# Optimization experiments

Hardware: AMD Instinct MI355X
Metric: run time of the kernel (lower is better)

## Reference

```python
import jax, jax.numpy as jnp
import numpy as np
from jax import lax

B, S, HDIM = 4, 2048, 1024
H, D, L = 16, 64, 128
NB = S // L
EPS = 1e-8


def setup_inputs() -> dict:
    key = jax.random.key(0)
    ks = jax.random.split(key, 16)
    std = 0.02
    inp = {
        'f_in': jax.random.normal(ks[0], (B, S, HDIM), jnp.float32),
        'i_in': jax.random.normal(ks[1], (B, S, HDIM), jnp.float32),
        'z_in': jax.random.normal(ks[2], (B, S, HDIM), jnp.float32),
        'o_in': jax.random.normal(ks[3], (B, S, HDIM), jnp.float32),
        'c0': jax.random.normal(ks[4], (B, H, D), jnp.float32),
        'h0': jax.random.normal(ks[5], (B, H, D), jnp.float32),
        # weights stored (in, out) so forward is x @ W + b
        'Wf': std * jax.random.normal(ks[6], (HDIM, H * D), jnp.float32),
        'bf': jnp.zeros((H * D,), jnp.float32),
        'Wi': std * jax.random.normal(ks[7], (HDIM, H * D), jnp.float32),
        'bi': jnp.zeros((H * D,), jnp.float32),
        'Wz': std * jax.random.normal(ks[8], (HDIM, H * D), jnp.float32),
        'bz': jnp.zeros((H * D,), jnp.float32),
        'Wo': std * jax.random.normal(ks[9], (HDIM, H * D), jnp.float32),
        'bo': jnp.zeros((H * D,), jnp.float32),
        'Wp': std * jax.random.normal(ks[10], (H * D, HDIM), jnp.float32),
        'bp': jnp.zeros((HDIM,), jnp.float32),
    }
    return inp


def _to_blocks(x):
    # (B,S,H*D) -> (NB, B, H, D, L), matching torch view+permute(1,0,3,4,2)
    return jnp.transpose(x.reshape(B, NB, L, H, D), (1, 0, 3, 4, 2))


def _qlstm(f_in, i_in, z_in, o_in, c0, Wf, bf, Wi, bi, Wz, bz, Wo, bo, Wp, bp):
    fx = _to_blocks(f_in @ Wf + bf)
    ix = _to_blocks(i_in @ Wi + bi)
    zx = _to_blocks(z_in @ Wz + bz)
    ox = _to_blocks(o_in @ Wo + bo)

    f = jax.nn.sigmoid(fx + 1.0)              # (NB,B,H,D,L)
    o = jax.nn.sigmoid(ox)
    update = jax.nn.sigmoid(ix) * jnp.tanh(zx)

    kk = jnp.arange(L)[:, None]
    ll = jnp.arange(L + 1)[None, :]
    ones_mask = ll >= kk + 1                   # (L, L+1): filled with 1.0
    zeros_mask = ll >= kk + 2                  # (L, L+1): zeroed out

    def block_step(c, blk):
        fb, ob, ub = blk                       # each (B,H,D,L)
        cf = jnp.concatenate([fb, jnp.ones(fb.shape[:-1] + (1,), fb.dtype)], axis=-1)  # (B,H,D,L+1)
        Fm = jnp.broadcast_to(cf[..., None, :], fb.shape[:-1] + (L, L + 1))
        Fm = jnp.where(ones_mask, 1.0, Fm)
        # reversed log-cumsum-exp along last axis (decay products)
        Fm = jnp.exp(jnp.flip(jnp.cumsum(jnp.flip(jnp.log(Fm + EPS), -1), -1), -1)) - EPS
        Fm = jnp.where(zeros_mask, 0.0, Fm)    # (B,H,D,L,L+1)
        u = jnp.concatenate([c[..., None], ub], axis=-1)   # (B,H,D,L+1)
        cs = jnp.einsum('bhdkl,bhdl->bhdk', Fm, u)          # (B,H,D,L)
        hs = ob * jnp.tanh(cs)
        return cs[..., -1], hs

    last_c, hs = lax.scan(block_step, c0, (f, o, update))   # hs: (NB,B,H,D,L)
    last_h = hs[-1, ..., -1]
    y = jnp.transpose(hs, (1, 0, 4, 2, 3)).reshape(B, S, H * D)
    y = y @ Wp + bp                            # (B,S,HDIM)
    return y, last_c, last_h


def reference(f_in, i_in, z_in, o_in, c0, h0, Wf, bf, Wi, bi, Wz, bz, Wo, bo, Wp, bp):
    y, last_c, last_h = _qlstm(f_in, i_in, z_in, o_in, c0,
                               Wf, bf, Wi, bi, Wz, bz, Wo, bo, Wp, bp)
    return y, last_c, last_h
```

## Files before the change

kernel.cpp:

```cpp
#include <hip/hip_runtime.h>
#include <hip/hip_bf16.h>
#include <stdint.h>

constexpr int GM = 8192;
constexpr int GK = 1024;
constexpr int GN = 1024;
constexpr size_t NACT = (size_t)GM * GN;
constexpr int CHUNK = 32;
constexpr int NCHUNK = 64;
constexpr int NCH = 4096;

#define DEVINL __device__ __forceinline__

typedef __attribute__((ext_vector_type(8))) short bf16x8;
typedef __attribute__((ext_vector_type(4))) float f32x4;

DEVINL float sigmoidf_(float x) { return 1.0f / (1.0f + __expf(-x)); }

DEVINL unsigned short f2bf(float x) {
  unsigned int u = __builtin_bit_cast(unsigned int, x);
  unsigned int rnd = 0x7fffu + ((u >> 16) & 1u);
  return (unsigned short)((u + rnd) >> 16);
}
DEVINL float bf2f(unsigned short u) {
  unsigned int x = ((unsigned int)u) << 16;
  return __builtin_bit_cast(float, x);
}

DEVINL void gload16(const void* g, void* l) {
  __builtin_amdgcn_global_load_lds(
      (const __attribute__((address_space(1))) unsigned int*)g,
      (__attribute__((address_space(3))) unsigned int*)l, 16, 0, 0);
}

__global__ void cvt_bf16_kernel(const float* __restrict__ src,
                                unsigned short* __restrict__ dst, int n4) {
  int i = blockIdx.x * blockDim.x + threadIdx.x;
  int stride = gridDim.x * blockDim.x;
  for (; i < n4; i += stride) {
    float4 v = ((const float4*)src)[i];
    ushort4 o;
    o.x = f2bf(v.x); o.y = f2bf(v.y); o.z = f2bf(v.z); o.w = f2bf(v.w);
    ((ushort4*)dst)[i] = o;
  }
}

__global__ void transpose_cvt_kernel(const float* __restrict__ W,
                                     unsigned short* __restrict__ Wt) {
  __shared__ float tile[32][33];
  int n0 = blockIdx.x * 32, k0 = blockIdx.y * 32;
  int tx = threadIdx.x & 31, ty = threadIdx.x >> 5;
#pragma unroll
  for (int i = 0; i < 32; i += 8)
    tile[ty + i][tx] = W[(size_t)(k0 + ty + i) * GN + n0 + tx];
  __syncthreads();
#pragma unroll
  for (int i = 0; i < 32; i += 8)
    Wt[(size_t)(n0 + ty + i) * GK + k0 + tx] = f2bf(tile[tx][ty + i]);
}

template <int MODE>
__global__ __launch_bounds__(256) void gemm128(
    const unsigned short* __restrict__ A1, const unsigned short* __restrict__ W1,
    const float* __restrict__ bias1,
    const unsigned short* __restrict__ A2, const unsigned short* __restrict__ W2,
    const float* __restrict__ bias2,
    unsigned short* __restrict__ outb, float* __restrict__ outf) {
  __shared__ __align__(16) unsigned short As[128 * 32];
  __shared__ __align__(16) unsigned short Bs[128 * 32];
  const int tid = threadIdx.x;
  const int wave = tid >> 6, lane = tid & 63;
  const int bm = blockIdx.x, bn = blockIdx.y;
  const int wm = (wave >> 1) * 64, wn = (wave & 1) * 64;
  const int lrow = lane & 15, lko = (lane >> 4) * 8;
  const int srow = tid >> 2, scol = (tid & 3) * 8;

  f32x4 acc1[4][4];
  f32x4 acc2[4][4];
#pragma unroll
  for (int m = 0; m < 4; ++m)
#pragma unroll
    for (int n = 0; n < 4; ++n) {
      acc1[m][n] = (f32x4){0.f, 0.f, 0.f, 0.f};
      acc2[m][n] = (f32x4){0.f, 0.f, 0.f, 0.f};
    }

  auto run = [&](const unsigned short* __restrict__ A,
                 const unsigned short* __restrict__ W, f32x4(&acc)[4][4]) {
    for (int k0 = 0; k0 < GK; k0 += 32) {
      __syncthreads();
      gload16(A + (size_t)(bm * 128 + srow) * GK + k0 + scol,
              (char*)As + wave * 1024);
      gload16(A + (size_t)(bm * 128 + 64 + srow) * GK + k0 + scol,
              (char*)As + 4096 + wave * 1024);
      gload16(W + (size_t)(bn * 128 + srow) * GK + k0 + scol,
              (char*)Bs + wave * 1024);
      gload16(W + (size_t)(bn * 128 + 64 + srow) * GK + k0 + scol,
              (char*)Bs + 4096 + wave * 1024);
      __syncthreads();

      bf16x8 af[4], bfr[4];
#pragma unroll
      for (int m = 0; m < 4; ++m)
        af[m] = *(const bf16x8*)&As[(wm + m * 16 + lrow) * 32 + lko];
#pragma unroll
      for (int n = 0; n < 4; ++n)
        bfr[n] = *(const bf16x8*)&Bs[(wn + n * 16 + lrow) * 32 + lko];
#pragma unroll
      for (int m = 0; m < 4; ++m)
#pragma unroll
        for (int n = 0; n < 4; ++n)
          acc[m][n] = __builtin_amdgcn_mfma_f32_16x16x32_bf16(af[m], bfr[n],
                                                              acc[m][n], 0, 0, 0);
    }
  };

  run(A1, W1, acc1);
  if constexpr (MODE == 2) run(A2, W2, acc2);

  float b1v[4], b2v[4];
#pragma unroll
  for (int n = 0; n < 4; ++n) {
    int gc = bn * 128 + wn + n * 16 + lrow;
    b1v[n] = bias1[gc];
    if constexpr (MODE == 2) b2v[n] = bias2[gc];
    else b2v[n] = 0.f;
  }

#pragma unroll
  for (int m = 0; m < 4; ++m) {
#pragma unroll
    for (int n = 0; n < 4; ++n) {
      int gc = bn * 128 + wn + n * 16 + lrow;
#pragma unroll
      for (int j = 0; j < 4; ++j) {
        int gr = bm * 128 + wm + m * 16 + (lane >> 4) * 4 + j;
        float v = acc1[m][n][j] + b1v[n];
        size_t oidx = (size_t)gr * GN + gc;
        if constexpr (MODE == 0) {
          outb[oidx] = f2bf(sigmoidf_(v + 1.0f));
        } else if constexpr (MODE == 1) {
          outb[oidx] = f2bf(sigmoidf_(v));
        } else if constexpr (MODE == 2) {
          float v2 = acc2[m][n][j] + b2v[n];
          outb[oidx] = f2bf(sigmoidf_(v) * tanhf(v2));
        } else {
          outf[oidx] = v;
        }
      }
    }
  }
}

__global__ void scan_phaseA_kernel(const unsigned short* __restrict__ F,
                                   const unsigned short* __restrict__ U,
                                   float* __restrict__ Pt, float* __restrict__ Ct) {
  int tid = blockIdx.x * blockDim.x + threadIdx.x;
  int ch = tid & (NCH - 1), chunk = tid >> 12;
  int b = ch >> 10, n = ch & 1023;
  size_t base = ((size_t)(b * 2048 + chunk * CHUNK)) * 1024 + n;
  float c = 0.f, P = 1.f;
#pragma unroll 8
  for (int t = 0; t < CHUNK; ++t) {
    size_t idx = base + (size_t)t * 1024;
    float f = bf2f(F[idx]);
    float u = bf2f(U[idx]);
    c = __builtin_fmaf(f, c, u);
    P *= f;
  }
  Pt[tid] = P;
  Ct[tid] = c;
}

__global__ void scan_combine_kernel(const float* __restrict__ Pt,
                                    const float* __restrict__ Ct,
                                    const float* __restrict__ c0,
                                    float* __restrict__ Cin,
                                    float* __restrict__ last_c) {
  int ch = blockIdx.x * blockDim.x + threadIdx.x;
  float c = c0[ch];
#pragma unroll
  for (int j = 0; j < NCHUNK; ++j) {
    Cin[j * NCH + ch] = c;
    c = __builtin_fmaf(Pt[j * NCH + ch], c, Ct[j * NCH + ch]);
  }
  last_c[ch] = c;
}

__global__ void scan_phaseC_kernel(const unsigned short* __restrict__ F,
                                   const unsigned short* __restrict__ U,
                                   const unsigned short* __restrict__ O,
                                   const float* __restrict__ Cin,
                                   unsigned short* __restrict__ Hb,
                                   float* __restrict__ last_h) {
  int tid = blockIdx.x * blockDim.x + threadIdx.x;
  int ch = tid & (NCH - 1), chunk = tid >> 12;
  int b = ch >> 10, n = ch & 1023;
  size_t base = ((size_t)(b * 2048 + chunk * CHUNK)) * 1024 + n;
  float c = Cin[tid];
  float h = 0.f;
#pragma unroll 8
  for (int t = 0; t < CHUNK; ++t) {
    size_t idx = base + (size_t)t * 1024;
    float f = bf2f(F[idx]);
    float u = bf2f(U[idx]);
    float o = bf2f(O[idx]);
    c = __builtin_fmaf(f, c, u);
    h = o * tanhf(c);
    Hb[idx] = f2bf(h);
  }
  if (chunk == NCHUNK - 1) last_h[ch] = h;
}

extern "C" void kernel_launch(void* const* d_in, const int* in_sizes, int n_in,
                              void* d_out, int out_size, void* d_ws, size_t ws_size,
                              hipStream_t stream) {
  const float* f_in = (const float*)d_in[0];
  const float* i_in = (const float*)d_in[1];
  const float* z_in = (const float*)d_in[2];
  const float* o_in = (const float*)d_in[3];
  const float* c0 = (const float*)d_in[4];
  const float* Wf = (const float*)d_in[6];
  const float* bf_ = (const float*)d_in[7];
  const float* Wi = (const float*)d_in[8];
  const float* bi = (const float*)d_in[9];
  const float* Wz = (const float*)d_in[10];
  const float* bz = (const float*)d_in[11];
  const float* Wo = (const float*)d_in[12];
  const float* bo = (const float*)d_in[13];
  const float* Wp = (const float*)d_in[14];
  const float* bp = (const float*)d_in[15];

  float* y = (float*)d_out;
  float* last_c = y + NACT;
  float* last_h = last_c + NCH;

  char* w = (char*)d_ws;
  const size_t ABYTES = NACT * 2;
  const size_t WBYTES = (size_t)GK * GN * 2;
  unsigned short* Af = (unsigned short*)(w + 0 * ABYTES);
  unsigned short* Ai = (unsigned short*)(w + 1 * ABYTES);
  unsigned short* Az = (unsigned short*)(w + 2 * ABYTES);
  unsigned short* Ao = (unsigned short*)(w + 3 * ABYTES);
  char* wt = w + 4 * ABYTES;
  unsigned short* Wtf = (unsigned short*)(wt + 0 * WBYTES);
  unsigned short* Wti = (unsigned short*)(wt + 1 * WBYTES);
  unsigned short* Wtz = (unsigned short*)(wt + 2 * WBYTES);
  unsigned short* Wto = (unsigned short*)(wt + 3 * WBYTES);
  unsigned short* Wtp = (unsigned short*)(wt + 4 * WBYTES);
  char* gp = wt + 5 * WBYTES;
  unsigned short* F = (unsigned short*)(gp + 0 * ABYTES);
  unsigned short* U = (unsigned short*)(gp + 1 * ABYTES);
  unsigned short* O = (unsigned short*)(gp + 2 * ABYTES);
  unsigned short* Hb = (unsigned short*)(gp + 3 * ABYTES);
  char* sp = gp + 4 * ABYTES;
  const size_t SBYTES = (size_t)NCH * NCHUNK * 4;
  float* Pt = (float*)(sp + 0 * SBYTES);
  float* Ct = (float*)(sp + 1 * SBYTES);
  float* Cin = (float*)(sp + 2 * SBYTES);

  const int n4 = (int)(NACT / 4);
  cvt_bf16_kernel<<<2048, 256, 0, stream>>>(f_in, Af, n4);
  cvt_bf16_kernel<<<2048, 256, 0, stream>>>(i_in, Ai, n4);
  cvt_bf16_kernel<<<2048, 256, 0, stream>>>(z_in, Az, n4);
  cvt_bf16_kernel<<<2048, 256, 0, stream>>>(o_in, Ao, n4);

  dim3 tg(32, 32);
  transpose_cvt_kernel<<<tg, 256, 0, stream>>>(Wf, Wtf);
  transpose_cvt_kernel<<<tg, 256, 0, stream>>>(Wi, Wti);
  transpose_cvt_kernel<<<tg, 256, 0, stream>>>(Wz, Wtz);
  transpose_cvt_kernel<<<tg, 256, 0, stream>>>(Wo, Wto);
  transpose_cvt_kernel<<<tg, 256, 0, stream>>>(Wp, Wtp);

  dim3 gg(GM / 128, GN / 128);
  gemm128<0><<<gg, 256, 0, stream>>>(Af, Wtf, bf_, nullptr, nullptr, nullptr, F, nullptr);
  gemm128<1><<<gg, 256, 0, stream>>>(Ao, Wto, bo, nullptr, nullptr, nullptr, O, nullptr);
  gemm128<2><<<gg, 256, 0, stream>>>(Ai, Wti, bi, Az, Wtz, bz, U, nullptr);

  scan_phaseA_kernel<<<(NCH * NCHUNK) / 256, 256, 0, stream>>>(F, U, Pt, Ct);
  scan_combine_kernel<<<NCH / 256, 256, 0, stream>>>(Pt, Ct, c0, Cin, last_c);
  scan_phaseC_kernel<<<(NCH * NCHUNK) / 256, 256, 0, stream>>>(F, U, O, Cin, Hb, last_h);

  gemm128<3><<<gg, 256, 0, stream>>>(Hb, Wtp, bp, nullptr, nullptr, nullptr, nullptr, y);
}
```

Baseline: 238.7 us.

## Replace GEMMs with 256x256 double-buffered swizzled MFMA kernel and batch launches

Replaces the 128x128 single-buffered GEMM with a 256x256-tile, 512-thread kernel. It double-buffers 64-wide K slices in LDS using XOR-swizzled layout, interleaves fragment loads with MFMA phases, and raises wave priority during MFMA. The four gate GEMMs now run as one launch over a z-dimension, and the sigmoid*tanh for the update gate moves into the two scan kernels, which read separate I and Z buffers. The conversion and transpose kernels are batched into single launches, and Hb reuses the Af buffer. The cost is 128KB of dynamic LDS, more register pressure, and the update activation being recomputed in both scan phases.

```diff
diff --git a/kernel.cpp b/kernel.cpp
--- a/kernel.cpp
+++ b/kernel.cpp
@@ -9,6 +9,7 @@
 constexpr int CHUNK = 32;
 constexpr int NCHUNK = 64;
 constexpr int NCH = 4096;
+constexpr int NT = GK / 64;
 
 #define DEVINL __device__ __forceinline__
 
@@ -33,20 +34,36 @@
       (__attribute__((address_space(3))) unsigned int*)l, 16, 0, 0);
 }
 
-__global__ void cvt_bf16_kernel(const float* __restrict__ src,
-                                unsigned short* __restrict__ dst, int n4) {
-  int i = blockIdx.x * blockDim.x + threadIdx.x;
+__global__ void cvt4_kernel(const float* __restrict__ s0, const float* __restrict__ s1,
+                            const float* __restrict__ s2, const float* __restrict__ s3,
+                            unsigned short* __restrict__ d0, unsigned short* __restrict__ d1,
+                            unsigned short* __restrict__ d2, unsigned short* __restrict__ d3,
+                            int n4) {
+  const float* s;
+  unsigned short* d;
+  switch (blockIdx.y) {
+    case 0: s = s0; d = d0; break;
+    case 1: s = s1; d = d1; break;
+    case 2: s = s2; d = d2; break;
+    default: s = s3; d = d3; break;
+  }
   int stride = gridDim.x * blockDim.x;
-  for (; i < n4; i += stride) {
-    float4 v = ((const float4*)src)[i];
+  for (int i = blockIdx.x * blockDim.x + threadIdx.x; i < n4; i += stride) {
+    float4 v = ((const float4*)s)[i];
     ushort4 o;
     o.x = f2bf(v.x); o.y = f2bf(v.y); o.z = f2bf(v.z); o.w = f2bf(v.w);
-    ((ushort4*)dst)[i] = o;
-  }
-}
-
-__global__ void transpose_cvt_kernel(const float* __restrict__ W,
-                                     unsigned short* __restrict__ Wt) {
+    ((ushort4*)d)[i] = o;
+  }
+}
+
+struct TPtrs {
+  const float* src[5];
+  unsigned short* dst[5];
+};
+
+__global__ void transpose_cvt_all(TPtrs p) {
+  const float* __restrict__ W = p.src[blockIdx.z];
+  unsigned short* __restrict__ Wt = p.dst[blockIdx.z];
   __shared__ float tile[32][33];
   int n0 = blockIdx.x * 32, k0 = blockIdx.y * 32;
   int tx = threadIdx.x & 31, ty = threadIdx.x >> 5;
@@ -59,101 +76,219 @@
     Wt[(size_t)(n0 + ty + i) * GK + k0 + tx] = f2bf(tile[tx][ty + i]);
 }
 
-template <int MODE>
-__global__ __launch_bounds__(256) void gemm128(
-    const unsigned short* __restrict__ A1, const unsigned short* __restrict__ W1,
-    const float* __restrict__ bias1,
-    const unsigned short* __restrict__ A2, const unsigned short* __restrict__ W2,
-    const float* __restrict__ bias2,
-    unsigned short* __restrict__ outb, float* __restrict__ outf) {
-  __shared__ __align__(16) unsigned short As[128 * 32];
-  __shared__ __align__(16) unsigned short Bs[128 * 32];
+DEVINL void gemm256_core(const unsigned short* __restrict__ A,
+                         const unsigned short* __restrict__ W,
+                         char* lds, int tid, int wave, int lane,
+                         int bm, int bn, f32x4 (&acc)[8][4]) {
+  const char* Ag = (const char*)A;
+  const char* Wg = (const char*)W;
+  const int Ah = wave >> 2;
+  const int wn = (wave & 3) * 64;
+  const int lrow = lane & 15;
+  const int lgrp = lane >> 4;
+
+  auto stage = [&](int buf, int tk) {
+#pragma unroll
+    for (int hh = 0; hh < 4; ++hh) {
+#pragma unroll
+      for (int j = 0; j < 2; ++j) {
+        const int lbyte = j * 8192 + tid * 16;
+        const int row = lbyte >> 7;
+        const int gcb = (lbyte & 127) ^ ((row & 7) << 4);
+        const char* src = (hh < 2)
+            ? Ag + (size_t)(bm * 256 + hh * 128 + row) * 2048 + tk * 128 + gcb
+            : Wg + (size_t)(bn * 256 + (hh - 2) * 128 + row) * 2048 + tk * 128 + gcb;
+        char* dst = lds + buf * 65536 + (hh >= 2 ? 32768 : 0) + (hh & 1) * 16384 +
+                    j * 8192 + wave * 1024;
+        gload16(src, dst);
+      }
+    }
+  };
+
+  stage(0, 0);
+
+  for (int t = 0; t < NT; ++t) {
+    const int cur = t & 1;
+    const char* Abase = lds + cur * 65536 + Ah * 16384;
+    const char* Bbase = lds + cur * 65536 + 32768;
+
+    stage(cur ^ 1, t + 1);
+    asm volatile("s_waitcnt vmcnt(8)" ::: "memory");
+    __builtin_amdgcn_sched_barrier(0);
+    __builtin_amdgcn_s_barrier();
+    __builtin_amdgcn_sched_barrier(0);
+
+    bf16x8 aF[4][2], bF[4][2];
+#pragma unroll
+    for (int m = 0; m < 4; ++m)
+#pragma unroll
+      for (int ks = 0; ks < 2; ++ks) {
+        const int r = m * 16 + lrow;
+        const int cb = ks * 64 + lgrp * 16;
+        aF[m][ks] = *(const bf16x8*)(Abase + r * 128 + (cb ^ ((r & 7) << 4)));
+      }
+#pragma unroll
+    for (int n = 0; n < 2; ++n)
+#pragma unroll
+      for (int ks = 0; ks < 2; ++ks) {
+        const int nr = wn + n * 16 + lrow;
+        const int cb = ks * 64 + lgrp * 16;
+        bF[n][ks] = *(const bf16x8*)(Bbase + nr * 128 + (cb ^ ((nr & 7) << 4)));
+      }
+    __builtin_amdgcn_s_setprio(1);
+#pragma unroll
+    for (int m = 0; m < 4; ++m)
+#pragma unroll
+      for (int n = 0; n < 2; ++n)
+#pragma unroll
+        for (int ks = 0; ks < 2; ++ks)
+          acc[m][n] = __builtin_amdgcn_mfma_f32_16x16x32_bf16(aF[m][ks], bF[n][ks],
+                                                              acc[m][n], 0, 0, 0);
+    __builtin_amdgcn_s_setprio(0);
+    __builtin_amdgcn_sched_barrier(0);
+    __builtin_amdgcn_s_barrier();
+    __builtin_amdgcn_sched_barrier(0);
+
+#pragma unroll
+    for (int n = 2; n < 4; ++n)
+#pragma unroll
+      for (int ks = 0; ks < 2; ++ks) {
+        const int nr = wn + n * 16 + lrow;
+        const int cb = ks * 64 + lgrp * 16;
+        bF[n][ks] = *(const bf16x8*)(Bbase + nr * 128 + (cb ^ ((nr & 7) << 4)));
+      }
+    __builtin_amdgcn_s_setprio(1);
+#pragma unroll
+    for (int m = 0; m < 4; ++m)
+#pragma unroll
+      for (int n = 2; n < 4; ++n)
+#pragma unroll
+        for (int ks = 0; ks < 2; ++ks)
+          acc[m][n] = __builtin_amdgcn_mfma_f32_16x16x32_bf16(aF[m][ks], bF[n][ks],
+                                                              acc[m][n], 0, 0, 0);
+    __builtin_amdgcn_s_setprio(0);
+    __builtin_amdgcn_sched_barrier(0);
+    __builtin_amdgcn_s_barrier();
+    __builtin_amdgcn_sched_barrier(0);
+
+#pragma unroll
+    for (int m = 0; m < 4; ++m)
+#pragma unroll
+      for (int ks = 0; ks < 2; ++ks) {
+        const int r = (m + 4) * 16 + lrow;
+        const int cb = ks * 64 + lgrp * 16;
+        aF[m][ks] = *(const bf16x8*)(Abase + r * 128 + (cb ^ ((r & 7) << 4)));
+      }
+    __builtin_amdgcn_s_setprio(1);
+#pragma unroll
+    for (int m = 0; m < 4; ++m)
+#pragma unroll
+      for (int n = 2; n < 4; ++n)
+#pragma unroll
+        for (int ks = 0; ks < 2; ++ks)
+          acc[m + 4][n] = __builtin_amdgcn_mfma_f32_16x16x32_bf16(aF[m][ks], bF[n][ks],
+                                                                  acc[m + 4][n], 0, 0, 0);
+    __builtin_amdgcn_s_setprio(0);
+    __builtin_amdgcn_sched_barrier(0);
+    __builtin_amdgcn_s_barrier();
+    __builtin_amdgcn_sched_barrier(0);
+
+    __builtin_amdgcn_s_setprio(1);
+#pragma unroll
+    for (int m = 0; m < 4; ++m)
+#pragma unroll
+      for (int n = 0; n < 2; ++n)
+#pragma unroll
+        for (int ks = 0; ks < 2; ++ks)
+          acc[m + 4][n] = __builtin_amdgcn_mfma_f32_16x16x32_bf16(aF[m][ks], bF[n][ks],
+                                                                  acc[m + 4][n], 0, 0, 0);
+    __builtin_amdgcn_s_setprio(0);
+  }
+}
+
+struct GateArgs {
+  const unsigned short* A[4];
+  const unsigned short* W[4];
+  const float* bias[4];
+  unsigned short* out[4];
+};
+
+__global__ __launch_bounds__(512, 2) void gemm_gates8(GateArgs ga) {
+  extern __shared__ char lds[];
+  const int tid = threadIdx.x;
+  const int wave = tid >> 6, lane = tid & 63;
+  const int bm = blockIdx.x, bn = blockIdx.y, gz = blockIdx.z;
+  const int wm = (wave >> 2) * 128, wn = (wave & 3) * 64;
+  const int lrow = lane & 15, lgrp = lane >> 4;
+
+  f32x4 acc[8][4];
+#pragma unroll
+  for (int m = 0; m < 8; ++m)
+#pragma unroll
+    for (int n = 0; n < 4; ++n) acc[m][n] = (f32x4){0.f, 0.f, 0.f, 0.f};
+
+  gemm256_core(ga.A[gz], ga.W[gz], lds, tid, wave, lane, bm, bn, acc);
+
+  const float* bias = ga.bias[gz];
+  unsigned short* out = ga.out[gz];
+  float bv[4];
+#pragma unroll
+  for (int n = 0; n < 4; ++n) bv[n] = bias[bn * 256 + wn + n * 16 + lrow];
+
+#pragma unroll
+  for (int m = 0; m < 8; ++m)
+#pragma unroll
+    for (int n = 0; n < 4; ++n) {
+      const int gc = bn * 256 + wn + n * 16 + lrow;
+#pragma unroll
+      for (int j = 0; j < 4; ++j) {
+        const int gr = bm * 256 + wm + m * 16 + lgrp * 4 + j;
+        float v = acc[m][n][j] + bv[n];
+        if (gz == 0) v = sigmoidf_(v + 1.0f);
+        else if (gz == 1) v = sigmoidf_(v);
+        out[(size_t)gr * GN + gc] = f2bf(v);
+      }
+    }
+}
+
+__global__ __launch_bounds__(512, 2) void gemm_proj8(
+    const unsigned short* __restrict__ A, const unsigned short* __restrict__ W,
+    const float* __restrict__ bias, float* __restrict__ out) {
+  extern __shared__ char lds[];
   const int tid = threadIdx.x;
   const int wave = tid >> 6, lane = tid & 63;
   const int bm = blockIdx.x, bn = blockIdx.y;
-  const int wm = (wave >> 1) * 64, wn = (wave & 1) * 64;
-  const int lrow = lane & 15, lko = (lane >> 4) * 8;
-  const int srow = tid >> 2, scol = (tid & 3) * 8;
-
-  f32x4 acc1[4][4];
-  f32x4 acc2[4][4];
-#pragma unroll
-  for (int m = 0; m < 4; ++m)
+  const int wm = (wave >> 2) * 128, wn = (wave & 3) * 64;
+  const int lrow = lane & 15, lgrp = lane >> 4;
+
+  f32x4 acc[8][4];
+#pragma unroll
+  for (int m = 0; m < 8; ++m)
+#pragma unroll
+    for (int n = 0; n < 4; ++n) acc[m][n] = (f32x4){0.f, 0.f, 0.f, 0.f};
+
+  gemm256_core(A, W, lds, tid, wave, lane, bm, bn, acc);
+
+  float bv[4];
+#pragma unroll
+  for (int n = 0; n < 4; ++n) bv[n] = bias[bn * 256 + wn + n * 16 + lrow];
+
+#pragma unroll
+  for (int m = 0; m < 8; ++m)
 #pragma unroll
     for (int n = 0; n < 4; ++n) {
-      acc1[m][n] = (f32x4){0.f, 0.f, 0.f, 0.f};
-      acc2[m][n] = (f32x4){0.f, 0.f, 0.f, 0.f};
+      const int gc = bn * 256 + wn + n * 16 + lrow;
+#pragma unroll
+      for (int j = 0; j < 4; ++j) {
+        const int gr = bm * 256 + wm + m * 16 + lgrp * 4 + j;
+        out[(size_t)gr * GN + gc] = acc[m][n][j] + bv[n];
+      }
     }
-
-  auto run = [&](const unsigned short* __restrict__ A,
-                 const unsigned short* __restrict__ W, f32x4(&acc)[4][4]) {
-    for (int k0 = 0; k0 < GK; k0 += 32) {
-      __syncthreads();
-      gload16(A + (size_t)(bm * 128 + srow) * GK + k0 + scol,
-              (char*)As + wave * 1024);
-      gload16(A + (size_t)(bm * 128 + 64 + srow) * GK + k0 + scol,
-              (char*)As + 4096 + wave * 1024);
-      gload16(W + (size_t)(bn * 128 + srow) * GK + k0 + scol,
-              (char*)Bs + wave * 1024);
-      gload16(W + (size_t)(bn * 128 + 64 + srow) * GK + k0 + scol,
-              (char*)Bs + 4096 + wave * 1024);
-      __syncthreads();
-
-      bf16x8 af[4], bfr[4];
-#pragma unroll
-      for (int m = 0; m < 4; ++m)
-        af[m] = *(const bf16x8*)&As[(wm + m * 16 + lrow) * 32 + lko];
-#pragma unroll
-      for (int n = 0; n < 4; ++n)
-        bfr[n] = *(const bf16x8*)&Bs[(wn + n * 16 + lrow) * 32 + lko];
-#pragma unroll
-      for (int m = 0; m < 4; ++m)
-#pragma unroll
-        for (int n = 0; n < 4; ++n)
-          acc[m][n] = __builtin_amdgcn_mfma_f32_16x16x32_bf16(af[m], bfr[n],
-                                                              acc[m][n], 0, 0, 0);
-    }
-  };
-
-  run(A1, W1, acc1);
-  if constexpr (MODE == 2) run(A2, W2, acc2);
-
-  float b1v[4], b2v[4];
-#pragma unroll
-  for (int n = 0; n < 4; ++n) {
-    int gc = bn * 128 + wn + n * 16 + lrow;
-    b1v[n] = bias1[gc];
-    if constexpr (MODE == 2) b2v[n] = bias2[gc];
-    else b2v[n] = 0.f;
-  }
-
-#pragma unroll
-  for (int m = 0; m < 4; ++m) {
-#pragma unroll
-    for (int n = 0; n < 4; ++n) {
-      int gc = bn * 128 + wn + n * 16 + lrow;
-#pragma unroll
-      for (int j = 0; j < 4; ++j) {
-        int gr = bm * 128 + wm + m * 16 + (lane >> 4) * 4 + j;
-        float v = acc1[m][n][j] + b1v[n];
-        size_t oidx = (size_t)gr * GN + gc;
-        if constexpr (MODE == 0) {
-          outb[oidx] = f2bf(sigmoidf_(v + 1.0f));
-        } else if constexpr (MODE == 1) {
-          outb[oidx] = f2bf(sigmoidf_(v));
-        } else if constexpr (MODE == 2) {
-          float v2 = acc2[m][n][j] + b2v[n];
-          outb[oidx] = f2bf(sigmoidf_(v) * tanhf(v2));
-        } else {
-          outf[oidx] = v;
-        }
-      }
-    }
-  }
 }
 
 __global__ void scan_phaseA_kernel(const unsigned short* __restrict__ F,
-                                   const unsigned short* __restrict__ U,
+                                   const unsigned short* __restrict__ Ip,
+                                   const unsigned short* __restrict__ Zp,
                                    float* __restrict__ Pt, float* __restrict__ Ct) {
   int tid = blockIdx.x * blockDim.x + threadIdx.x;
   int ch = tid & (NCH - 1), chunk = tid >> 12;
@@ -164,7 +299,7 @@
   for (int t = 0; t < CHUNK; ++t) {
     size_t idx = base + (size_t)t * 1024;
     float f = bf2f(F[idx]);
-    float u = bf2f(U[idx]);
+    float u = sigmoidf_(bf2f(Ip[idx])) * tanhf(bf2f(Zp[idx]));
     c = __builtin_fmaf(f, c, u);
     P *= f;
   }
@@ -188,7 +323,8 @@
 }
 
 __global__ void scan_phaseC_kernel(const unsigned short* __restrict__ F,
-                                   const unsigned short* __restrict__ U,
+                                   const unsigned short* __restrict__ Ip,
+                                   const unsigned short* __restrict__ Zp,
                                    const unsigned short* __restrict__ O,
                                    const float* __restrict__ Cin,
                                    unsigned short* __restrict__ Hb,
@@ -203,7 +339,7 @@
   for (int t = 0; t < CHUNK; ++t) {
     size_t idx = base + (size_t)t * 1024;
     float f = bf2f(F[idx]);
-    float u = bf2f(U[idx]);
+    float u = sigmoidf_(bf2f(Ip[idx])) * tanhf(bf2f(Zp[idx]));
     float o = bf2f(O[idx]);
     c = __builtin_fmaf(f, c, u);
     h = o * tanhf(c);
@@ -250,36 +386,40 @@
   unsigned short* Wtp = (unsigned short*)(wt + 4 * WBYTES);
   char* gp = wt + 5 * WBYTES;
   unsigned short* F = (unsigned short*)(gp + 0 * ABYTES);
-  unsigned short* U = (unsigned short*)(gp + 1 * ABYTES);
-  unsigned short* O = (unsigned short*)(gp + 2 * ABYTES);
-  unsigned short* Hb = (unsigned short*)(gp + 3 * ABYTES);
+  unsigned short* O = (unsigned short*)(gp + 1 * ABYTES);
+  unsigned short* Ip = (unsigned short*)(gp + 2 * ABYTES);
+  unsigned short* Zp = (unsigned short*)(gp + 3 * ABYTES);
+  unsigned short* Hb = Af;
   char* sp = gp + 4 * ABYTES;
   const size_t SBYTES = (size_t)NCH * NCHUNK * 4;
   float* Pt = (float*)(sp + 0 * SBYTES);
   float* Ct = (float*)(sp + 1 * SBYTES);
   float* Cin = (float*)(sp + 2 * SBYTES);
 
-  const int n4 = (int)(NACT / 4);
-  cvt_bf16_kernel<<<2048, 256, 0, stream>>>(f_in, Af, n4);
-  cvt_bf16_kernel<<<2048, 256, 0, stream>>>(i_in, Ai, n4);
-  cvt_bf16_kernel<<<2048, 256, 0, stream>>>(z_in, Az, n4);
-  cvt_bf16_kernel<<<2048, 256, 0, stream>>>(o_in, Ao, n4);
-
-  dim3 tg(32, 32);
-  transpose_cvt_kernel<<<tg, 256, 0, stream>>>(Wf, Wtf);
-  transpose_cvt_kernel<<<tg, 256, 0, stream>>>(Wi, Wti);
-  transpose_cvt_kernel<<<tg, 256, 0, stream>>>(Wz, Wtz);
-  transpose_cvt_kernel<<<tg, 256, 0, stream>>>(Wo, Wto);
-  transpose_cvt_kernel<<<tg, 256, 0, stream>>>(Wp, Wtp);
-
-  dim3 gg(GM / 128, GN / 128);
-  gemm128<0><<<gg, 256, 0, stream>>>(Af, Wtf, bf_, nullptr, nullptr, nullptr, F, nullptr);
-  gemm128<1><<<gg, 256, 0, stream>>>(Ao, Wto, bo, nullptr, nullptr, nullptr, O, nullptr);
-  gemm128<2><<<gg, 256, 0, stream>>>(Ai, Wti, bi, Az, Wtz, bz, U, nullptr);
-
-  scan_phaseA_kernel<<<(NCH * NCHUNK) / 256, 256, 0, stream>>>(F, U, Pt, Ct);
+  (void)hipFuncSetAttribute((const void*)gemm_gates8,
+                            hipFuncAttributeMaxDynamicSharedMemorySize, 131072);
+  (void)hipFuncSetAttribute((const void*)gemm_proj8,
+                            hipFuncAttributeMaxDynamicSharedMemorySize, 131072);
+
+  cvt4_kernel<<<dim3(1024, 4), 256, 0, stream>>>(
+      f_in, o_in, i_in, z_in, Af, Ao, Ai, Az, (int)(NACT / 4));
+
+  TPtrs tp;
+  tp.src[0] = Wf; tp.src[1] = Wi; tp.src[2] = Wz; tp.src[3] = Wo; tp.src[4] = Wp;
+  tp.dst[0] = Wtf; tp.dst[1] = Wti; tp.dst[2] = Wtz; tp.dst[3] = Wto; tp.dst[4] = Wtp;
+  transpose_cvt_all<<<dim3(32, 32, 5), 256, 0, stream>>>(tp);
+
+  GateArgs ga;
+  ga.A[0] = Af;  ga.A[1] = Ao;  ga.A[2] = Ai;  ga.A[3] = Az;
+  ga.W[0] = Wtf; ga.W[1] = Wto; ga.W[2] = Wti; ga.W[3] = Wtz;
+  ga.bias[0] = bf_; ga.bias[1] = bo; ga.bias[2] = bi; ga.bias[3] = bz;
+  ga.out[0] = F; ga.out[1] = O; ga.out[2] = Ip; ga.out[3] = Zp;
+  gemm_gates8<<<dim3(GM / 256, GN / 256, 4), 512, 131072, stream>>>(ga);
+
+  scan_phaseA_kernel<<<(NCH * NCHUNK) / 256, 256, 0, stream>>>(F, Ip, Zp, Pt, Ct);
   scan_combine_kernel<<<NCH / 256, 256, 0, stream>>>(Pt, Ct, c0, Cin, last_c);
-  scan_phaseC_kernel<<<(NCH * NCHUNK) / 256, 256, 0, stream>>>(F, U, O, Cin, Hb, last_h);
-
-  gemm128<3><<<gg, 256, 0, stream>>>(Hb, Wtp, bp, nullptr, nullptr, nullptr, nullptr, y);
-}
+  scan_phaseC_kernel<<<(NCH * NCHUNK) / 256, 256, 0, stream>>>(F, Ip, Zp, O, Cin, Hb,
+                                                               last_h);
+
+  gemm_proj8<<<dim3(GM / 256, GN / 256), 512, 131072, stream>>>(Hb, Wtp, bp, y);
+}
```

Result: faster. 217.2 us (-9.0%).
